# Performance work log

Measured on AMD Instinct MI355X. Metric: run time of the kernel, lower is better.

The kernel has to match this reference:

```python
import jax, jax.numpy as jnp
import numpy as np

B, S, C, D, V = 64, 128, 32, 512, 20000

def setup_inputs() -> dict:
    key = jax.random.key(0)
    ks = jax.random.split(key, 16)
    sc = 1.0 / np.sqrt(D)
    emb = jax.random.normal(ks[0], (V + 1, D), jnp.float32) * 0.02
    emb = emb.at[V].set(0.0)  # padding_idx=-1 -> last row zero
    inp = dict(
        emb=emb,
        W_all_w=jax.random.uniform(ks[1], (4 * D, D), jnp.float32, -sc, sc),
        W_all_b=jnp.zeros((4 * D,), jnp.float32),
        U_all_w=jax.random.uniform(ks[2], (4 * D, D), jnp.float32, -sc, sc),
        U_all_b=jnp.zeros((4 * D,), jnp.float32),
        W_d_w=jax.random.uniform(ks[3], (D, D), jnp.float32, -sc, sc),
        W_d_b=jnp.zeros((D,), jnp.float32),
        sel_w=jax.random.uniform(ks[4], (64, 1), jnp.float32, -1.0, 1.0),
        sel_b=jnp.zeros((64,), jnp.float32),
        time_w=jax.random.uniform(ks[5], (D, 64), jnp.float32, -0.125, 0.125),
        time_b=jnp.zeros((D,), jnp.float32),
        out_w=jax.random.uniform(ks[6], (2, D), jnp.float32, -sc, sc),
        out_b=jnp.zeros((2,), jnp.float32),
        seq_time_step=jax.random.uniform(ks[7], (B, S), jnp.float32, 0.0, 365.0),
        input_seqs=jax.random.randint(ks[8], (B, S, C), 0, V),
        mask=jnp.zeros((B, S), bool),
        lengths=jax.random.randint(ks[9], (B,), 1, S),
        codemask=jnp.zeros((B, S, C), bool),
        label=jax.random.randint(ks[10], (B,), 0, 2),
    )
    return inp


def reference(emb, W_all_w, W_all_b, U_all_w, U_all_b, W_d_w, W_d_b,
              sel_w, sel_b, time_w, time_b, out_w, out_b, seq_time_step,
              input_seqs, mask, lengths, codemask, label):
    # visit embedding: sum code embeddings -> [B,S,D]
    x = emb[input_seqs].sum(axis=2)
    # time feature: 1 - tanh(selection_layer(t/180)^2) -> time_layer -> [B,S,D]
    t = (seq_time_step / 180.0)[..., None]                      # [B,S,1]
    tf = 1.0 - jnp.tanh(jnp.square(t * sel_w[:, 0] + sel_b))    # [B,S,64]
    tf = jnp.einsum('bsk,dk->bsd', tf, time_w) + time_b         # [B,S,D]
    # precompute input projection for all steps: [B,S,4D]
    ux = jnp.einsum('bsd,ed->bse', x, U_all_w) + U_all_b

    def step(carry, inputs):
        h, c = carry
        tf_s, ux_s = inputs                                      # [B,D], [B,4D]
        c_s1 = jnp.tanh(c @ W_d_w.T + W_d_b)
        c_adj = c - c_s1 + c_s1 * tf_s
        outs = h @ W_all_w.T + W_all_b + ux_s
        f, i, o, c_tmp = jnp.split(jax.nn.sigmoid(outs), 4, axis=1)
        c_new = f * c_adj + i * c_tmp
        h_new = o * jnp.tanh(c_new)
        return (h_new, c_new), h_new

    h0 = jnp.zeros((B, D), x.dtype)
    c0 = jnp.zeros((B, D), x.dtype)
    tf_t = jnp.swapaxes(tf, 0, 1)   # [S,B,D]
    ux_t = jnp.swapaxes(ux, 0, 1)   # [S,B,4D]
    _, hs = jax.lax.scan(step, (h0, c0), (tf_t, ux_t))
    outputs = jnp.swapaxes(hs, 0, 1)           # [B,S,D]
    pooled = outputs.max(axis=1)                # MaxPoolLayer without mask
    out = pooled @ out_w.T + out_b              # [B,2]
    return out
```

## Files before the change

kernel.cpp:

```cpp
#include <hip/hip_runtime.h>
#include <hip/hip_bf16.h>

#define B_ 64
#define S_ 128
#define C_ 32
#define D_ 512
#define V_ 20000

typedef float     f32x4  __attribute__((ext_vector_type(4)));
typedef _Float16  f16x8  __attribute__((ext_vector_type(8)));

#define AS1 __attribute__((address_space(1)))
#define AS3 __attribute__((address_space(3)))

#define OFF_XH   0ull
#define OFF_UH   8388608ull
#define OFF_AW   10485760ull
#define OFF_CB   13631488ull
#define OFF_PAD  13639680ull
#define OFF_TWT  13647872ull
#define OFF_EMBH 13778944ull
#define OFF_TF   34259968ull
#define OFF_UX   42648576ull
#define OFF_XB2  76203008ull

#define SENT32 0x7FFF7FFFu

__global__ void k_prep_fused(
    const float* __restrict__ outb, float* __restrict__ outv,
    int4* __restrict__ fillp,
    const float* __restrict__ Wallb, const float* __restrict__ Uallb,
    float* __restrict__ cb,
    const float* __restrict__ tw, float* __restrict__ twt,
    const float* __restrict__ U, _Float16* __restrict__ uh,
    const float* __restrict__ Wall, const float* __restrict__ Wd,
    int4* __restrict__ AW,
    const float* __restrict__ emb, _Float16* __restrict__ eh)
{
    const int blk = blockIdx.x;
    const int t   = threadIdx.x;
    if (blk < 1) {
        if (t < 128) outv[t] = outb[t & 1];
    } else if (blk < 4097) {
        fillp[(blk - 1) * 256 + t] =
            int4{(int)SENT32, (int)SENT32, (int)SENT32, (int)SENT32};
    } else if (blk < 4098) {
        #pragma unroll
        for (int k = 0; k < 8; k++) {
            int i = t * 8 + k;
            cb[i] = Wallb[i] + Uallb[i];
        }
    } else if (blk < 4130) {
        int i2 = (blk - 4098) * 256 + t;
        #pragma unroll
        for (int k = 0; k < 4; k++) {
            int i = i2 * 4 + k;
            twt[(i & 63) * 512 + (i >> 6)] = tw[i];
        }
    } else if (blk < 5154) {
        int i = (blk - 4130) * 256 + t;
        float4 v = ((const float4*)U)[i];
        union { _Float16 h[4]; unsigned long long u; } pk;
        pk.h[0] = (_Float16)v.x; pk.h[1] = (_Float16)v.y;
        pk.h[2] = (_Float16)v.z; pk.h[3] = (_Float16)v.w;
        ((unsigned long long*)uh)[i] = pk.u;
    } else if (blk < 5922) {
        int i = (blk - 5154) * 256 + t;
        int lane = i & 63;  int r = i >> 6;
        int kt = r & 15;    r >>= 4;
        int tile = r % 3;   r /= 3;
        int w = r & 7;      int m = r >> 3;
        int row16 = lane & 15, quad = lane >> 4;
        int q = tile * 2 + (row16 >> 3);
        int d = m * 64 + w * 8 + (row16 & 7);
        int k0 = kt * 32 + quad * 8;
        union { _Float16 h[8]; int4 v; } u;
        const float* src = nullptr;
        if (q < 4)       src = Wall + (size_t)(q * 512 + d) * 512 + k0;
        else if (q == 4) src = Wd   + (size_t)d * 512 + k0;
        #pragma unroll
        for (int j = 0; j < 8; j++) u.h[j] = src ? (_Float16)src[j] : (_Float16)0.f;
        AW[i] = u.v;
    } else {
        int i = (blk - 5922) * 256 + t;
        float2 v = ((const float2*)emb)[i];
        unsigned short hx = __builtin_bit_cast(unsigned short, (_Float16)v.x);
        unsigned short hy = __builtin_bit_cast(unsigned short, (_Float16)v.y);
        ((unsigned*)eh)[i] = (unsigned)hx | ((unsigned)hy << 16);
    }
}

__global__ void k_embed2(const _Float16* __restrict__ embh, const int* __restrict__ seqs,
                         _Float16* __restrict__ xh)
{
    int bs = blockIdx.x;
    int t  = threadIdx.x;
    __shared__ int rows[32];
    if (t < 32) {
        int r = seqs[(size_t)bs * C_ + t];
        rows[t] = (r < 0) ? V_ : r;
    }
    __syncthreads();
    float ax = 0.f, ay = 0.f;
    #pragma unroll 4
    for (int c = 0; c < C_; c++) {
        unsigned v = *(const unsigned*)(embh + (size_t)rows[c] * D_ + 2 * t);
        ax += (float)__builtin_bit_cast(_Float16, (unsigned short)v);
        ay += (float)__builtin_bit_cast(_Float16, (unsigned short)(v >> 16));
    }
    unsigned short hx = __builtin_bit_cast(unsigned short, (_Float16)ax);
    unsigned short hy = __builtin_bit_cast(unsigned short, (_Float16)ay);
    *(unsigned*)(xh + (size_t)bs * D_ + 2 * t) = (unsigned)hx | ((unsigned)hy << 16);
}

__global__ __launch_bounds__(512) void k_tf2(
    const float* __restrict__ stime, const float* __restrict__ selw,
    const float* __restrict__ selb, const float* __restrict__ twT,
    const float* __restrict__ timeb, _Float16* __restrict__ tf)
{
    int bb = blockIdx.x;
    int t  = threadIdx.x;
    __shared__ float s1[16][64];
    for (int idx = t; idx < 1024; idx += 512) {
        int bl = idx >> 6, j = idx & 63;
        float tv = stime[bb * 16 + bl] * (1.0f / 180.0f);
        float u  = tv * selw[j] + selb[j];
        s1[bl][j] = 1.0f - tanhf(u * u);
    }
    __syncthreads();
    int d = t;
    float acc[16];
    float tb = timeb[d];
    #pragma unroll
    for (int l = 0; l < 16; l++) acc[l] = tb;
    for (int j = 0; j < 64; j++) {
        float wj = twT[j * 512 + d];
        #pragma unroll
        for (int l = 0; l < 16; l++) acc[l] = fmaf(s1[l][j], wj, acc[l]);
    }
    #pragma unroll
    for (int l = 0; l < 16; l++)
        tf[(size_t)(bb * 16 + l) * 512 + d] = (_Float16)acc[l];
}

__device__ __forceinline__ void stage16(const _Float16* g, _Float16* l)
{
#if __has_builtin(__builtin_amdgcn_global_load_lds)
    __builtin_amdgcn_global_load_lds((const AS1 void*)g, (AS3 void*)l, 16, 0, 0);
#else
    *(int4*)l = *(const int4*)g;
#endif
}

__global__ __launch_bounds__(256, 4) void k_gemm3(const _Float16* __restrict__ A,
                                                  const _Float16* __restrict__ Bm,
                                                  _Float16* __restrict__ Cg)
{
    __shared__ __align__(16) _Float16 As[128 * 64];
    __shared__ __align__(16) _Float16 Bs[128 * 64];
    const int t = threadIdx.x;
    const int w = t >> 6, lane = t & 63;
    const int wm = w & 1, wn = w >> 1;
    const int m0 = blockIdx.y * 128, n0 = blockIdx.x * 128;
    const int r16 = lane & 15, quad = lane >> 4;

    const int srow = w * 8 + (lane >> 3);
    const int k8g  = (lane & 7) ^ ((lane >> 3) & 7);
    const _Float16* ga = A  + (size_t)(m0 + srow) * 512 + k8g * 8;
    const _Float16* gb = Bm + (size_t)(n0 + srow) * 512 + k8g * 8;
    _Float16* la = As + srow * 64 + (lane & 7) * 8;
    _Float16* lb = Bs + srow * 64 + (lane & 7) * 8;

    f32x4 acc[4][4] = {};
    for (int k0 = 0; k0 < 512; k0 += 64) {
        __syncthreads();
        #pragma unroll
        for (int r = 0; r < 4; r++) {
            stage16(ga + k0 + (size_t)r * 32 * 512, la + r * 32 * 64);
            stage16(gb + k0 + (size_t)r * 32 * 512, lb + r * 32 * 64);
        }
        __syncthreads();
        #pragma unroll
        for (int sub = 0; sub < 2; sub++) {
            f16x8 af[4], bf[4];
            const int ksl = ((sub * 4 + quad) ^ (r16 & 7)) * 8;
            #pragma unroll
            for (int i = 0; i < 4; i++) {
                af[i] = *(const f16x8*)(As + (wm * 64 + i * 16 + r16) * 64 + ksl);
                bf[i] = *(const f16x8*)(Bs + (wn * 64 + i * 16 + r16) * 64 + ksl);
            }
            #pragma unroll
            for (int i = 0; i < 4; i++)
                #pragma unroll
                for (int j = 0; j < 4; j++)
                    acc[i][j] = __builtin_amdgcn_mfma_f32_16x16x32_f16(
                                    af[i], bf[j], acc[i][j], 0, 0, 0);
        }
    }
    #pragma unroll
    for (int i = 0; i < 4; i++)
        #pragma unroll
        for (int j = 0; j < 4; j++) {
            int row = m0 + wm * 64 + i * 16 + quad * 4;
            int col = n0 + wn * 64 + j * 16 + r16;
            _Float16* cp = Cg + (size_t)row * 2048 + col;
            #pragma unroll
            for (int rg = 0; rg < 4; rg++)
                cp[(size_t)rg * 2048] = (_Float16)acc[i][j][rg];
        }
}

__device__ __forceinline__ float fsigm(float x)
{
    return __builtin_amdgcn_rcpf(1.f + __expf(-x));
}
__device__ __forceinline__ float ftanh(float x)
{
    return 1.f - 2.f * __builtin_amdgcn_rcpf(1.f + __expf(2.f * x));
}

__global__ __launch_bounds__(512, 2) void k_rnn7(
    const int4* __restrict__ AW,
    const float* __restrict__ cbv, const float* __restrict__ wdb,
    const _Float16* __restrict__ ux, const _Float16* __restrict__ tf,
    const float* __restrict__ outw,
    float* __restrict__ out,
    unsigned long long* __restrict__ xb64)
{
    const int t    = threadIdx.x;
    const int gid  = blockIdx.x >> 3;
    const int m    = blockIdx.x & 7;
    const int b0   = gid * 2;
    const int w    = t >> 6;
    const int lane = t & 63;
    const int col  = lane & 15;
    const int quad = lane >> 4;

    int4 Af[48];
    {
        const int4* src = AW + (size_t)(m * 8 + w) * 3072;
        #pragma unroll
        for (int i = 0; i < 48; i++) Af[i] = src[i * 64 + lane];
    }

    __shared__ __align__(16) _Float16 xstg[4 * 544];
    __shared__ __align__(16) float cmat[8][4][48];
    __shared__ float pstg[2][64];

    const bool act = (lane < 16);
    const int  pb  = lane >> 3;
    const int  pj  = lane & 7;
    const int  dl  = w * 8 + pj;
    const int  d   = m * 64 + dl;

    float cbf = 0, cbi = 0, cbo = 0, cbc = 0, bdv = 0;
    if (act) {
        cbf = cbv[d]; cbi = cbv[512 + d]; cbo = cbv[1024 + d]; cbc = cbv[1536 + d];
        bdv = wdb[d];
    }
    float c_reg = 0.f, pool = -1e30f;
    const int dw = w * 64 + lane;

    for (int s = 0; s < S_; s++) {
        float uf = 0, ui = 0, uo = 0, uc = 0, tv = 0;
        if (act) {
            size_t bs = (size_t)(b0 + pb) * S_ + s;
            const _Float16* up = ux + bs * 2048 + d;
            uf = (float)up[0];    ui = (float)up[512];
            uo = (float)up[1024]; uc = (float)up[1536];
            tv = (float)tf[bs * 512 + d];
        }

        unsigned long long val = 0ull;
        if (s > 0) {
            const unsigned long long* src =
                xb64 + (((size_t)s * 32 + gid) * 8 + w) * 64 + lane;
            int tries = 0;
            for (;;) {
                val = __hip_atomic_load(src, __ATOMIC_RELAXED,
                                        __HIP_MEMORY_SCOPE_AGENT);
                if ((unsigned)val != SENT32 && (unsigned)(val >> 32) != SENT32)
                    break;
                if (++tries > (1 << 22)) break;
            }
        }
        __syncthreads();
        xstg[0 * 544 + dw] = __builtin_bit_cast(_Float16, (unsigned short)(val));
        xstg[2 * 544 + dw] = __builtin_bit_cast(_Float16, (unsigned short)(val >> 16));
        xstg[1 * 544 + dw] = __builtin_bit_cast(_Float16, (unsigned short)(val >> 32));
        xstg[3 * 544 + dw] = __builtin_bit_cast(_Float16, (unsigned short)(val >> 48));
        __syncthreads();

        f32x4 a0 = {0, 0, 0, 0}, a1 = {0, 0, 0, 0}, a2 = {0, 0, 0, 0};
        #pragma unroll
        for (int kt = 0; kt < 16; kt++) {
            f16x8 b = {};
            if (col < 4)
                b = *(const f16x8*)(xstg + col * 544 + kt * 32 + quad * 8);
            a0 = __builtin_amdgcn_mfma_f32_16x16x32_f16(
                     __builtin_bit_cast(f16x8, Af[kt]),      b, a0, 0, 0, 0);
            a1 = __builtin_amdgcn_mfma_f32_16x16x32_f16(
                     __builtin_bit_cast(f16x8, Af[16 + kt]), b, a1, 0, 0, 0);
            a2 = __builtin_amdgcn_mfma_f32_16x16x32_f16(
                     __builtin_bit_cast(f16x8, Af[32 + kt]), b, a2, 0, 0, 0);
        }

        if (col < 4) {
            *(f32x4*)&cmat[w][col][ 0 + quad * 4] = a0;
            *(f32x4*)&cmat[w][col][16 + quad * 4] = a1;
            *(f32x4*)&cmat[w][col][32 + quad * 4] = a2;
        }

        if (act) {
            float f_  = cmat[w][pb][ 0 + pj];
            float i_  = cmat[w][pb][ 8 + pj];
            float o_  = cmat[w][pb][16 + pj];
            float g_  = cmat[w][pb][24 + pj];
            float wd_ = cmat[w][2 + pb][32 + pj];
            float gf = fsigm(f_ + cbf + uf);
            float gi = fsigm(i_ + cbi + ui);
            float go = fsigm(o_ + cbo + uo);
            float gc = fsigm(g_ + cbc + uc);
            float cs1  = ftanh(wd_ + bdv);
            float cadj = c_reg - cs1 + cs1 * tv;
            float cn   = gf * cadj + gi * gc;
            float hn   = go * ftanh(cn);
            c_reg = cn;
            pool  = fmaxf(pool, hn);
            unsigned hh = __builtin_bit_cast(unsigned short, (_Float16)hn);
            unsigned cc = __builtin_bit_cast(unsigned short, (_Float16)cn);
            unsigned pk = hh | (cc << 16);
            unsigned other = __shfl(pk, lane + 8);
            if (pb == 0 && s != S_ - 1) {
                unsigned long long ov =
                    (unsigned long long)pk | ((unsigned long long)other << 32);
                unsigned long long* dst =
                    xb64 + (((size_t)(s + 1) * 32 + gid) * 8 + m) * 64 + dl;
                __hip_atomic_store(dst, ov, __ATOMIC_RELAXED,
                                   __HIP_MEMORY_SCOPE_AGENT);
            }
        }
    }

    if (act) pstg[pb][dl] = pool;
    __syncthreads();
    if (t < 128) {
        int b = t >> 6, l = t & 63;
        float pv = pstg[b][l];
        int dg = m * 64 + l;
        float p0 = pv * outw[dg], p1 = pv * outw[512 + dg];
        #pragma unroll
        for (int off = 32; off > 0; off >>= 1) {
            p0 += __shfl_down(p0, off);
            p1 += __shfl_down(p1, off);
        }
        if (l == 0) {
            atomicAdd(&out[2 * (b0 + b)],     p0);
            atomicAdd(&out[2 * (b0 + b) + 1], p1);
        }
    }
}

extern "C" void kernel_launch(void* const* d_in, const int* in_sizes, int n_in,
                              void* d_out, int out_size, void* d_ws, size_t ws_size,
                              hipStream_t stream)
{
    const float* emb   = (const float*)d_in[0];
    const float* Wall  = (const float*)d_in[1];
    const float* Wallb = (const float*)d_in[2];
    const float* Uall  = (const float*)d_in[3];
    const float* Uallb = (const float*)d_in[4];
    const float* Wdw   = (const float*)d_in[5];
    const float* Wdb   = (const float*)d_in[6];
    const float* selw  = (const float*)d_in[7];
    const float* selb  = (const float*)d_in[8];
    const float* timew = (const float*)d_in[9];
    const float* timeb = (const float*)d_in[10];
    const float* outw  = (const float*)d_in[11];
    const float* outb  = (const float*)d_in[12];
    const float* stime = (const float*)d_in[13];
    const int*   seqs  = (const int*)d_in[14];
    float* out = (float*)d_out;
    char*  ws  = (char*)d_ws;

    _Float16* xh   = (_Float16*)(ws + OFF_XH);
    _Float16* uh   = (_Float16*)(ws + OFF_UH);
    int4*     aw   = (int4*)(ws + OFF_AW);
    float*    cbp  = (float*)(ws + OFF_CB);
    float*    twt  = (float*)(ws + OFF_TWT);
    _Float16* eh   = (_Float16*)(ws + OFF_EMBH);
    _Float16* tfp  = (_Float16*)(ws + OFF_TF);
    _Float16* uxp  = (_Float16*)(ws + OFF_UX);
    unsigned long long* xb = (unsigned long long*)(ws + OFF_XB2);

    k_prep_fused<<<25923, 256, 0, stream>>>(
        outb, out, (int4*)(ws + OFF_XB2),
        Wallb, Uallb, cbp,
        timew, twt,
        Uall, uh,
        Wall, Wdw, aw,
        emb, eh);
    k_embed2 <<<B_ * S_, 256, 0, stream>>>(eh, seqs, xh);
    k_tf2    <<<512,     512, 0, stream>>>(stime, selw, selb, twt, timeb, tfp);
    k_gemm3  <<<dim3(16, 64), 256, 0, stream>>>(xh, uh, uxp);
    k_rnn7   <<<256,     512, 0, stream>>>(aw, cbp, Wdb, uxp, tfp, outw, out, xb);
}
```

Before: 492.7 us.

## Process eight batch rows per RNN block and prefetch next-step hidden state

The recurrent kernel now handles 8 batch rows per block instead of 2, using all 16 MFMA columns, and launches 64 blocks instead of 256. Each thread issues the next step's cross-block state loads right after publishing its own output, overlapping the spin-wait latency with the tail of the current step. The ux/tf loads move after the barrier. This cuts the number of blocks that must synchronise through global memory and raises MFMA utilisation, at the cost of fewer CUs doing the recurrence and more per-step work per block.

```diff
diff --git a/kernel.cpp b/kernel.cpp
--- a/kernel.cpp
+++ b/kernel.cpp
@@ -219,7 +219,7 @@
     return 1.f - 2.f * __builtin_amdgcn_rcpf(1.f + __expf(2.f * x));
 }
 
-__global__ __launch_bounds__(512, 2) void k_rnn7(
+__global__ __launch_bounds__(512, 2) void k_rnn8(
     const int4* __restrict__ AW,
     const float* __restrict__ cbv, const float* __restrict__ wdb,
     const _Float16* __restrict__ ux, const _Float16* __restrict__ tf,
@@ -228,9 +228,8 @@
     unsigned long long* __restrict__ xb64)
 {
     const int t    = threadIdx.x;
-    const int gid  = blockIdx.x >> 3;
-    const int m    = blockIdx.x & 7;
-    const int b0   = gid * 2;
+    const int gp   = blockIdx.x & 7;
+    const int m    = blockIdx.x >> 3;
     const int w    = t >> 6;
     const int lane = t & 63;
     const int col  = lane & 15;
@@ -238,65 +237,81 @@
 
     int4 Af[48];
     {
-        const int4* src = AW + (size_t)(m * 8 + w) * 3072;
-        #pragma unroll
-        for (int i = 0; i < 48; i++) Af[i] = src[i * 64 + lane];
-    }
-
-    __shared__ __align__(16) _Float16 xstg[4 * 544];
-    __shared__ __align__(16) float cmat[8][4][48];
-    __shared__ float pstg[2][64];
-
-    const bool act = (lane < 16);
-    const int  pb  = lane >> 3;
-    const int  pj  = lane & 7;
-    const int  dl  = w * 8 + pj;
-    const int  d   = m * 64 + dl;
-
-    float cbf = 0, cbi = 0, cbo = 0, cbc = 0, bdv = 0;
-    if (act) {
-        cbf = cbv[d]; cbi = cbv[512 + d]; cbo = cbv[1024 + d]; cbc = cbv[1536 + d];
-        bdv = wdb[d];
-    }
+        const int4* srcA = AW + (size_t)(m * 8 + w) * 3072;
+        #pragma unroll
+        for (int i = 0; i < 48; i++) Af[i] = srcA[i * 64 + lane];
+    }
+
+    __shared__ __align__(16) _Float16 xstg[16 * 552];
+    __shared__ __align__(16) float cmat[8][16][52];
+    __shared__ float pstg[8][64];
+
+    const int pj = lane & 7;
+    const int bl = lane >> 3;
+    const int g  = bl >> 1;
+    const int pb = bl & 1;
+    const int dl = w * 8 + pj;
+    const int d  = m * 64 + dl;
+    const int hc = g * 4 + pb;
+    const int cc = g * 4 + 2 + pb;
+
+    const float cbf = cbv[d],        cbi = cbv[512 + d],
+                cbo = cbv[1024 + d], cbc = cbv[1536 + d];
+    const float bdv = wdb[d];
+
     float c_reg = 0.f, pool = -1e30f;
     const int dw = w * 64 + lane;
 
+    const size_t pbase = (size_t)gp * 2048 + (size_t)w * 64 + lane;
+    const size_t bs_base = (size_t)(gp * 8 + bl) * S_;
+
+    unsigned long long nx0 = 0, nx1 = 0, nx2 = 0, nx3 = 0;
+
     for (int s = 0; s < S_; s++) {
-        float uf = 0, ui = 0, uo = 0, uc = 0, tv = 0;
-        if (act) {
-            size_t bs = (size_t)(b0 + pb) * S_ + s;
-            const _Float16* up = ux + bs * 2048 + d;
-            uf = (float)up[0];    ui = (float)up[512];
-            uo = (float)up[1024]; uc = (float)up[1536];
-            tv = (float)tf[bs * 512 + d];
-        }
-
-        unsigned long long val = 0ull;
+        unsigned long long v0 = 0, v1 = 0, v2 = 0, v3 = 0;
         if (s > 0) {
-            const unsigned long long* src =
-                xb64 + (((size_t)s * 32 + gid) * 8 + w) * 64 + lane;
+            v0 = nx0; v1 = nx1; v2 = nx2; v3 = nx3;
+            const unsigned long long* sp = xb64 + (size_t)s * 16384 + pbase;
             int tries = 0;
-            for (;;) {
-                val = __hip_atomic_load(src, __ATOMIC_RELAXED,
-                                        __HIP_MEMORY_SCOPE_AGENT);
-                if ((unsigned)val != SENT32 && (unsigned)(val >> 32) != SENT32)
-                    break;
+            while (((unsigned)v0 == SENT32 || (unsigned)(v0 >> 32) == SENT32) ||
+                   ((unsigned)v1 == SENT32 || (unsigned)(v1 >> 32) == SENT32) ||
+                   ((unsigned)v2 == SENT32 || (unsigned)(v2 >> 32) == SENT32) ||
+                   ((unsigned)v3 == SENT32 || (unsigned)(v3 >> 32) == SENT32)) {
+                v0 = __hip_atomic_load(sp,        __ATOMIC_RELAXED, __HIP_MEMORY_SCOPE_AGENT);
+                v1 = __hip_atomic_load(sp + 512,  __ATOMIC_RELAXED, __HIP_MEMORY_SCOPE_AGENT);
+                v2 = __hip_atomic_load(sp + 1024, __ATOMIC_RELAXED, __HIP_MEMORY_SCOPE_AGENT);
+                v3 = __hip_atomic_load(sp + 1536, __ATOMIC_RELAXED, __HIP_MEMORY_SCOPE_AGENT);
                 if (++tries > (1 << 22)) break;
             }
         }
         __syncthreads();
-        xstg[0 * 544 + dw] = __builtin_bit_cast(_Float16, (unsigned short)(val));
-        xstg[2 * 544 + dw] = __builtin_bit_cast(_Float16, (unsigned short)(val >> 16));
-        xstg[1 * 544 + dw] = __builtin_bit_cast(_Float16, (unsigned short)(val >> 32));
-        xstg[3 * 544 + dw] = __builtin_bit_cast(_Float16, (unsigned short)(val >> 48));
+        xstg[ 0 * 552 + dw] = __builtin_bit_cast(_Float16, (unsigned short)(v0));
+        xstg[ 2 * 552 + dw] = __builtin_bit_cast(_Float16, (unsigned short)(v0 >> 16));
+        xstg[ 1 * 552 + dw] = __builtin_bit_cast(_Float16, (unsigned short)(v0 >> 32));
+        xstg[ 3 * 552 + dw] = __builtin_bit_cast(_Float16, (unsigned short)(v0 >> 48));
+        xstg[ 4 * 552 + dw] = __builtin_bit_cast(_Float16, (unsigned short)(v1));
+        xstg[ 6 * 552 + dw] = __builtin_bit_cast(_Float16, (unsigned short)(v1 >> 16));
+        xstg[ 5 * 552 + dw] = __builtin_bit_cast(_Float16, (unsigned short)(v1 >> 32));
+        xstg[ 7 * 552 + dw] = __builtin_bit_cast(_Float16, (unsigned short)(v1 >> 48));
+        xstg[ 8 * 552 + dw] = __builtin_bit_cast(_Float16, (unsigned short)(v2));
+        xstg[10 * 552 + dw] = __builtin_bit_cast(_Float16, (unsigned short)(v2 >> 16));
+        xstg[ 9 * 552 + dw] = __builtin_bit_cast(_Float16, (unsigned short)(v2 >> 32));
+        xstg[11 * 552 + dw] = __builtin_bit_cast(_Float16, (unsigned short)(v2 >> 48));
+        xstg[12 * 552 + dw] = __builtin_bit_cast(_Float16, (unsigned short)(v3));
+        xstg[14 * 552 + dw] = __builtin_bit_cast(_Float16, (unsigned short)(v3 >> 16));
+        xstg[13 * 552 + dw] = __builtin_bit_cast(_Float16, (unsigned short)(v3 >> 32));
+        xstg[15 * 552 + dw] = __builtin_bit_cast(_Float16, (unsigned short)(v3 >> 48));
         __syncthreads();
 
+        const _Float16* up = ux + (bs_base + s) * 2048 + d;
+        float uf = (float)up[0],    ui = (float)up[512];
+        float uo = (float)up[1024], uc = (float)up[1536];
+        float tv = (float)tf[(bs_base + s) * 512 + d];
+
         f32x4 a0 = {0, 0, 0, 0}, a1 = {0, 0, 0, 0}, a2 = {0, 0, 0, 0};
         #pragma unroll
         for (int kt = 0; kt < 16; kt++) {
-            f16x8 b = {};
-            if (col < 4)
-                b = *(const f16x8*)(xstg + col * 544 + kt * 32 + quad * 8);
+            f16x8 b = *(const f16x8*)(xstg + col * 552 + kt * 32 + quad * 8);
             a0 = __builtin_amdgcn_mfma_f32_16x16x32_f16(
                      __builtin_bit_cast(f16x8, Af[kt]),      b, a0, 0, 0, 0);
             a1 = __builtin_amdgcn_mfma_f32_16x16x32_f16(
@@ -304,59 +319,60 @@
             a2 = __builtin_amdgcn_mfma_f32_16x16x32_f16(
                      __builtin_bit_cast(f16x8, Af[32 + kt]), b, a2, 0, 0, 0);
         }
-
-        if (col < 4) {
-            *(f32x4*)&cmat[w][col][ 0 + quad * 4] = a0;
-            *(f32x4*)&cmat[w][col][16 + quad * 4] = a1;
-            *(f32x4*)&cmat[w][col][32 + quad * 4] = a2;
-        }
-
-        if (act) {
-            float f_  = cmat[w][pb][ 0 + pj];
-            float i_  = cmat[w][pb][ 8 + pj];
-            float o_  = cmat[w][pb][16 + pj];
-            float g_  = cmat[w][pb][24 + pj];
-            float wd_ = cmat[w][2 + pb][32 + pj];
-            float gf = fsigm(f_ + cbf + uf);
-            float gi = fsigm(i_ + cbi + ui);
-            float go = fsigm(o_ + cbo + uo);
-            float gc = fsigm(g_ + cbc + uc);
-            float cs1  = ftanh(wd_ + bdv);
-            float cadj = c_reg - cs1 + cs1 * tv;
-            float cn   = gf * cadj + gi * gc;
-            float hn   = go * ftanh(cn);
-            c_reg = cn;
-            pool  = fmaxf(pool, hn);
-            unsigned hh = __builtin_bit_cast(unsigned short, (_Float16)hn);
-            unsigned cc = __builtin_bit_cast(unsigned short, (_Float16)cn);
-            unsigned pk = hh | (cc << 16);
-            unsigned other = __shfl(pk, lane + 8);
-            if (pb == 0 && s != S_ - 1) {
-                unsigned long long ov =
-                    (unsigned long long)pk | ((unsigned long long)other << 32);
-                unsigned long long* dst =
-                    xb64 + (((size_t)(s + 1) * 32 + gid) * 8 + m) * 64 + dl;
-                __hip_atomic_store(dst, ov, __ATOMIC_RELAXED,
-                                   __HIP_MEMORY_SCOPE_AGENT);
-            }
-        }
-    }
-
-    if (act) pstg[pb][dl] = pool;
+        *(f32x4*)&cmat[w][col][ 0 + quad * 4] = a0;
+        *(f32x4*)&cmat[w][col][16 + quad * 4] = a1;
+        *(f32x4*)&cmat[w][col][32 + quad * 4] = a2;
+
+        float f_  = cmat[w][hc][ 0 + pj];
+        float i_  = cmat[w][hc][ 8 + pj];
+        float o_  = cmat[w][hc][16 + pj];
+        float g_  = cmat[w][hc][24 + pj];
+        float wd_ = cmat[w][cc][32 + pj];
+        float gf = fsigm(f_ + cbf + uf);
+        float gi = fsigm(i_ + cbi + ui);
+        float go = fsigm(o_ + cbo + uo);
+        float gc = fsigm(g_ + cbc + uc);
+        float cs1  = ftanh(wd_ + bdv);
+        float cadj = c_reg - cs1 + cs1 * tv;
+        float cn   = gf * cadj + gi * gc;
+        float hn   = go * ftanh(cn);
+        c_reg = cn;
+        pool  = fmaxf(pool, hn);
+        unsigned hh  = __builtin_bit_cast(unsigned short, (_Float16)hn);
+        unsigned chn = __builtin_bit_cast(unsigned short, (_Float16)cn);
+        unsigned pk  = hh | (chn << 16);
+        unsigned other = __shfl(pk, lane + 8);
+        if (pb == 0 && s != S_ - 1) {
+            unsigned long long ov =
+                (unsigned long long)pk | ((unsigned long long)other << 32);
+            unsigned long long* dst =
+                xb64 + (((size_t)(s + 1) * 32 + (gp * 4 + g)) * 8 + m) * 64 + dl;
+            __hip_atomic_store(dst, ov, __ATOMIC_RELAXED,
+                               __HIP_MEMORY_SCOPE_AGENT);
+        }
+        if (s + 1 < S_) {
+            const unsigned long long* np = xb64 + (size_t)(s + 1) * 16384 + pbase;
+            nx0 = __hip_atomic_load(np,        __ATOMIC_RELAXED, __HIP_MEMORY_SCOPE_AGENT);
+            nx1 = __hip_atomic_load(np + 512,  __ATOMIC_RELAXED, __HIP_MEMORY_SCOPE_AGENT);
+            nx2 = __hip_atomic_load(np + 1024, __ATOMIC_RELAXED, __HIP_MEMORY_SCOPE_AGENT);
+            nx3 = __hip_atomic_load(np + 1536, __ATOMIC_RELAXED, __HIP_MEMORY_SCOPE_AGENT);
+        }
+    }
+
+    pstg[bl][dl] = pool;
     __syncthreads();
-    if (t < 128) {
-        int b = t >> 6, l = t & 63;
-        float pv = pstg[b][l];
-        int dg = m * 64 + l;
+    {
+        float pv = pstg[w][lane];
+        int dg = m * 64 + lane;
         float p0 = pv * outw[dg], p1 = pv * outw[512 + dg];
         #pragma unroll
         for (int off = 32; off > 0; off >>= 1) {
             p0 += __shfl_down(p0, off);
             p1 += __shfl_down(p1, off);
         }
-        if (l == 0) {
-            atomicAdd(&out[2 * (b0 + b)],     p0);
-            atomicAdd(&out[2 * (b0 + b) + 1], p1);
+        if (lane == 0) {
+            atomicAdd(&out[2 * (gp * 8 + w)],     p0);
+            atomicAdd(&out[2 * (gp * 8 + w) + 1], p1);
         }
     }
 }
@@ -403,5 +419,5 @@
     k_embed2 <<<B_ * S_, 256, 0, stream>>>(eh, seqs, xh);
     k_tf2    <<<512,     512, 0, stream>>>(stime, selw, selb, twt, timeb, tfp);
     k_gemm3  <<<dim3(16, 64), 256, 0, stream>>>(xh, uh, uxp);
-    k_rnn7   <<<256,     512, 0, stream>>>(aw, cbp, Wdb, uxp, tfp, outw, out, xb);
-}
+    k_rnn8   <<<64,      512, 0, stream>>>(aw, cbp, Wdb, uxp, tfp, outw, out, xb);
+}
```

Measured after the change: 623.6 us. 26.6% more time.

## Repartition recurrent kernel: 8 batches per block, 16-row tiles, split-K warps

Applied to the files above, without the earlier changes.

The persistent RNN kernel is repartitioned. Before, each block owned 2 batches and 64 hidden units. Now each block owns 8 batches and 16 hidden units, with 10 warps, each covering one gate tile and one half of K. The MFMA B operand now uses all 16 columns (8 batches × h/c) instead of 4, so fewer wasted MFMA lanes and far fewer weight registers per warp (8 int4 instead of 48). The cost is an extra LDS reduction across the two K halves, wider polling loads of the exchange buffer per step, and one block per CU at 640 threads. The weight prep layout is changed to match, and padding tiles are removed.

```diff
diff --git a/kernel.cpp b/kernel.cpp
--- a/kernel.cpp
+++ b/kernel.cpp
@@ -64,25 +64,23 @@
         pk.h[0] = (_Float16)v.x; pk.h[1] = (_Float16)v.y;
         pk.h[2] = (_Float16)v.z; pk.h[3] = (_Float16)v.w;
         ((unsigned long long*)uh)[i] = pk.u;
-    } else if (blk < 5922) {
+    } else if (blk < 5794) {
         int i = (blk - 5154) * 256 + t;
         int lane = i & 63;  int r = i >> 6;
-        int kt = r & 15;    r >>= 4;
-        int tile = r % 3;   r /= 3;
-        int w = r & 7;      int m = r >> 3;
-        int row16 = lane & 15, quad = lane >> 4;
-        int q = tile * 2 + (row16 >> 3);
-        int d = m * 64 + w * 8 + (row16 & 7);
-        int k0 = kt * 32 + quad * 8;
+        int ktl   = r & 7;  int r2 = r >> 3;
+        int khalf = r2 & 1; int r3 = r2 >> 1;
+        int tile  = r3 % 5; int mm = r3 / 5;
+        int row16 = lane & 15, q4 = lane >> 4;
+        int d  = mm * 16 + row16;
+        int k0 = khalf * 256 + ktl * 32 + q4 * 8;
+        const float* src = (tile < 4) ? (Wall + (size_t)(tile * 512 + d) * 512 + k0)
+                                      : (Wd   + (size_t)d * 512 + k0);
         union { _Float16 h[8]; int4 v; } u;
-        const float* src = nullptr;
-        if (q < 4)       src = Wall + (size_t)(q * 512 + d) * 512 + k0;
-        else if (q == 4) src = Wd   + (size_t)d * 512 + k0;
-        #pragma unroll
-        for (int j = 0; j < 8; j++) u.h[j] = src ? (_Float16)src[j] : (_Float16)0.f;
+        #pragma unroll
+        for (int j = 0; j < 8; j++) u.h[j] = (_Float16)src[j];
         AW[i] = u.v;
     } else {
-        int i = (blk - 5922) * 256 + t;
+        int i = (blk - 5794) * 256 + t;
         float2 v = ((const float2*)emb)[i];
         unsigned short hx = __builtin_bit_cast(unsigned short, (_Float16)v.x);
         unsigned short hy = __builtin_bit_cast(unsigned short, (_Float16)v.y);
@@ -219,7 +217,7 @@
     return 1.f - 2.f * __builtin_amdgcn_rcpf(1.f + __expf(2.f * x));
 }
 
-__global__ __launch_bounds__(512, 2) void k_rnn7(
+__global__ __launch_bounds__(640, 1) void k_rnn9(
     const int4* __restrict__ AW,
     const float* __restrict__ cbv, const float* __restrict__ wdb,
     const _Float16* __restrict__ ux, const _Float16* __restrict__ tf,
@@ -228,95 +226,101 @@
     unsigned long long* __restrict__ xb64)
 {
     const int t    = threadIdx.x;
-    const int gid  = blockIdx.x >> 3;
-    const int m    = blockIdx.x & 7;
-    const int b0   = gid * 2;
+    const int g    = blockIdx.x >> 5;
+    const int mm   = blockIdx.x & 31;
     const int w    = t >> 6;
     const int lane = t & 63;
     const int col  = lane & 15;
     const int quad = lane >> 4;
-
-    int4 Af[48];
+    const int tile = w >> 1, khalf = w & 1;
+
+    int4 Af[8];
     {
-        const int4* src = AW + (size_t)(m * 8 + w) * 3072;
-        #pragma unroll
-        for (int i = 0; i < 48; i++) Af[i] = src[i * 64 + lane];
-    }
-
-    __shared__ __align__(16) _Float16 xstg[4 * 544];
-    __shared__ __align__(16) float cmat[8][4][48];
-    __shared__ float pstg[2][64];
-
-    const bool act = (lane < 16);
-    const int  pb  = lane >> 3;
-    const int  pj  = lane & 7;
-    const int  dl  = w * 8 + pj;
-    const int  d   = m * 64 + dl;
+        const int4* src = AW + (size_t)(((mm * 5 + tile) * 2 + khalf) * 8) * 64;
+        #pragma unroll
+        for (int i = 0; i < 8; i++) Af[i] = src[i * 64 + lane];
+    }
+
+    __shared__ __align__(16) _Float16 xstg[16 * 520];
+    __shared__ __align__(16) float cmat[5][2][16][20];
+
+    const bool act = (t < 128);
+    const int bl   = t >> 4;
+    const int d16  = t & 15;
+    const int gg   = bl >> 1, pb = bl & 1;
+    const int dg   = mm * 16 + d16;
+    const int batch = g * 8 + bl;
+    const int hcol = gg * 4 + pb;
+    const int ccol = gg * 4 + 2 + pb;
 
     float cbf = 0, cbi = 0, cbo = 0, cbc = 0, bdv = 0;
     if (act) {
-        cbf = cbv[d]; cbi = cbv[512 + d]; cbo = cbv[1024 + d]; cbc = cbv[1536 + d];
-        bdv = wdb[d];
+        cbf = cbv[dg]; cbi = cbv[512 + dg]; cbo = cbv[1024 + dg]; cbc = cbv[1536 + dg];
+        bdv = wdb[dg];
     }
     float c_reg = 0.f, pool = -1e30f;
-    const int dw = w * 64 + lane;
+
+    const bool stg = (t < 512);
+    const int  k0  = (t * 4) & 511;
+    const int  sgg = t >> 7;
+    const size_t pboff = (size_t)g * 2048 + (size_t)t * 4;
 
     for (int s = 0; s < S_; s++) {
-        float uf = 0, ui = 0, uo = 0, uc = 0, tv = 0;
-        if (act) {
-            size_t bs = (size_t)(b0 + pb) * S_ + s;
-            const _Float16* up = ux + bs * 2048 + d;
-            uf = (float)up[0];    ui = (float)up[512];
-            uo = (float)up[1024]; uc = (float)up[1536];
-            tv = (float)tf[bs * 512 + d];
-        }
-
-        unsigned long long val = 0ull;
-        if (s > 0) {
-            const unsigned long long* src =
-                xb64 + (((size_t)s * 32 + gid) * 8 + w) * 64 + lane;
+        unsigned long long v0 = 0, v1 = 0, v2 = 0, v3 = 0;
+        if (stg && s > 0) {
+            const unsigned long long* sp = xb64 + (size_t)s * 16384 + pboff;
             int tries = 0;
             for (;;) {
-                val = __hip_atomic_load(src, __ATOMIC_RELAXED,
-                                        __HIP_MEMORY_SCOPE_AGENT);
-                if ((unsigned)val != SENT32 && (unsigned)(val >> 32) != SENT32)
+                v0 = __hip_atomic_load(sp + 0, __ATOMIC_RELAXED, __HIP_MEMORY_SCOPE_AGENT);
+                v1 = __hip_atomic_load(sp + 1, __ATOMIC_RELAXED, __HIP_MEMORY_SCOPE_AGENT);
+                v2 = __hip_atomic_load(sp + 2, __ATOMIC_RELAXED, __HIP_MEMORY_SCOPE_AGENT);
+                v3 = __hip_atomic_load(sp + 3, __ATOMIC_RELAXED, __HIP_MEMORY_SCOPE_AGENT);
+                if ((unsigned)v0 != SENT32 && (unsigned)v1 != SENT32 &&
+                    (unsigned)v2 != SENT32 && (unsigned)v3 != SENT32)
                     break;
                 if (++tries > (1 << 22)) break;
             }
         }
+        if (stg) {
+            unsigned long long h0 = (v0 & 0xFFFFull)         | ((v1 & 0xFFFFull) << 16)
+                                  | ((v2 & 0xFFFFull) << 32) | ((v3 & 0xFFFFull) << 48);
+            unsigned long long c0 = ((v0 >> 16) & 0xFFFFull)         | (((v1 >> 16) & 0xFFFFull) << 16)
+                                  | (((v2 >> 16) & 0xFFFFull) << 32) | (((v3 >> 16) & 0xFFFFull) << 48);
+            unsigned long long h1 = ((v0 >> 32) & 0xFFFFull)         | (((v1 >> 32) & 0xFFFFull) << 16)
+                                  | (((v2 >> 32) & 0xFFFFull) << 32) | (((v3 >> 32) & 0xFFFFull) << 48);
+            unsigned long long c1 = (v0 >> 48)          | ((v1 >> 48) << 16)
+                                  | ((v2 >> 48) << 32)  | ((v3 >> 48) << 48);
+            *(unsigned long long*)(xstg + (sgg * 4 + 0) * 520 + k0) = h0;
+            *(unsigned long long*)(xstg + (sgg * 4 + 1) * 520 + k0) = h1;
+            *(unsigned long long*)(xstg + (sgg * 4 + 2) * 520 + k0) = c0;
+            *(unsigned long long*)(xstg + (sgg * 4 + 3) * 520 + k0) = c1;
+        }
         __syncthreads();
-        xstg[0 * 544 + dw] = __builtin_bit_cast(_Float16, (unsigned short)(val));
-        xstg[2 * 544 + dw] = __builtin_bit_cast(_Float16, (unsigned short)(val >> 16));
-        xstg[1 * 544 + dw] = __builtin_bit_cast(_Float16, (unsigned short)(val >> 32));
-        xstg[3 * 544 + dw] = __builtin_bit_cast(_Float16, (unsigned short)(val >> 48));
+
+        float uf = 0, ui = 0, uo = 0, uc = 0, tv = 0;
+        if (act) {
+            const _Float16* up = ux + ((size_t)batch * S_ + s) * 2048 + dg;
+            uf = (float)up[0];    ui = (float)up[512];
+            uo = (float)up[1024]; uc = (float)up[1536];
+            tv = (float)tf[((size_t)batch * S_ + s) * 512 + dg];
+        }
+
+        f32x4 a = {0, 0, 0, 0};
+        #pragma unroll
+        for (int kt = 0; kt < 8; kt++) {
+            f16x8 b = *(const f16x8*)(xstg + col * 520 + (khalf * 8 + kt) * 32 + quad * 8);
+            a = __builtin_amdgcn_mfma_f32_16x16x32_f16(
+                    __builtin_bit_cast(f16x8, Af[kt]), b, a, 0, 0, 0);
+        }
+        *(f32x4*)&cmat[tile][khalf][col][quad * 4] = a;
         __syncthreads();
 
-        f32x4 a0 = {0, 0, 0, 0}, a1 = {0, 0, 0, 0}, a2 = {0, 0, 0, 0};
-        #pragma unroll
-        for (int kt = 0; kt < 16; kt++) {
-            f16x8 b = {};
-            if (col < 4)
-                b = *(const f16x8*)(xstg + col * 544 + kt * 32 + quad * 8);
-            a0 = __builtin_amdgcn_mfma_f32_16x16x32_f16(
-                     __builtin_bit_cast(f16x8, Af[kt]),      b, a0, 0, 0, 0);
-            a1 = __builtin_amdgcn_mfma_f32_16x16x32_f16(
-                     __builtin_bit_cast(f16x8, Af[16 + kt]), b, a1, 0, 0, 0);
-            a2 = __builtin_amdgcn_mfma_f32_16x16x32_f16(
-                     __builtin_bit_cast(f16x8, Af[32 + kt]), b, a2, 0, 0, 0);
-        }
-
-        if (col < 4) {
-            *(f32x4*)&cmat[w][col][ 0 + quad * 4] = a0;
-            *(f32x4*)&cmat[w][col][16 + quad * 4] = a1;
-            *(f32x4*)&cmat[w][col][32 + quad * 4] = a2;
-        }
-
         if (act) {
-            float f_  = cmat[w][pb][ 0 + pj];
-            float i_  = cmat[w][pb][ 8 + pj];
-            float o_  = cmat[w][pb][16 + pj];
-            float g_  = cmat[w][pb][24 + pj];
-            float wd_ = cmat[w][2 + pb][32 + pj];
+            float f_  = cmat[0][0][hcol][d16] + cmat[0][1][hcol][d16];
+            float i_  = cmat[1][0][hcol][d16] + cmat[1][1][hcol][d16];
+            float o_  = cmat[2][0][hcol][d16] + cmat[2][1][hcol][d16];
+            float g_  = cmat[3][0][hcol][d16] + cmat[3][1][hcol][d16];
+            float wd_ = cmat[4][0][ccol][d16] + cmat[4][1][ccol][d16];
             float gf = fsigm(f_ + cbf + uf);
             float gi = fsigm(i_ + cbi + ui);
             float go = fsigm(o_ + cbo + uo);
@@ -327,36 +331,31 @@
             float hn   = go * ftanh(cn);
             c_reg = cn;
             pool  = fmaxf(pool, hn);
-            unsigned hh = __builtin_bit_cast(unsigned short, (_Float16)hn);
-            unsigned cc = __builtin_bit_cast(unsigned short, (_Float16)cn);
-            unsigned pk = hh | (cc << 16);
-            unsigned other = __shfl(pk, lane + 8);
+            unsigned hh  = __builtin_bit_cast(unsigned short, (_Float16)hn);
+            unsigned chn = __builtin_bit_cast(unsigned short, (_Float16)cn);
+            unsigned pk  = hh | (chn << 16);
+            unsigned other = __shfl(pk, lane + 16);
             if (pb == 0 && s != S_ - 1) {
                 unsigned long long ov =
                     (unsigned long long)pk | ((unsigned long long)other << 32);
                 unsigned long long* dst =
-                    xb64 + (((size_t)(s + 1) * 32 + gid) * 8 + m) * 64 + dl;
+                    xb64 + (size_t)(s + 1) * 16384 + (size_t)(g * 4 + gg) * 512 + dg;
                 __hip_atomic_store(dst, ov, __ATOMIC_RELAXED,
                                    __HIP_MEMORY_SCOPE_AGENT);
             }
         }
     }
 
-    if (act) pstg[pb][dl] = pool;
-    __syncthreads();
-    if (t < 128) {
-        int b = t >> 6, l = t & 63;
-        float pv = pstg[b][l];
-        int dg = m * 64 + l;
-        float p0 = pv * outw[dg], p1 = pv * outw[512 + dg];
-        #pragma unroll
-        for (int off = 32; off > 0; off >>= 1) {
-            p0 += __shfl_down(p0, off);
-            p1 += __shfl_down(p1, off);
-        }
-        if (l == 0) {
-            atomicAdd(&out[2 * (b0 + b)],     p0);
-            atomicAdd(&out[2 * (b0 + b) + 1], p1);
+    if (act) {
+        float p0 = pool * outw[dg], p1 = pool * outw[512 + dg];
+        #pragma unroll
+        for (int off = 8; off > 0; off >>= 1) {
+            p0 += __shfl_down(p0, off, 16);
+            p1 += __shfl_down(p1, off, 16);
+        }
+        if (d16 == 0) {
+            atomicAdd(&out[2 * batch],     p0);
+            atomicAdd(&out[2 * batch + 1], p1);
         }
     }
 }
@@ -393,7 +392,7 @@
     _Float16* uxp  = (_Float16*)(ws + OFF_UX);
     unsigned long long* xb = (unsigned long long*)(ws + OFF_XB2);
 
-    k_prep_fused<<<25923, 256, 0, stream>>>(
+    k_prep_fused<<<25795, 256, 0, stream>>>(
         outb, out, (int4*)(ws + OFF_XB2),
         Wallb, Uallb, cbp,
         timew, twt,
@@ -403,5 +402,5 @@
     k_embed2 <<<B_ * S_, 256, 0, stream>>>(eh, seqs, xh);
     k_tf2    <<<512,     512, 0, stream>>>(stime, selw, selb, twt, timeb, tfp);
     k_gemm3  <<<dim3(16, 64), 256, 0, stream>>>(xh, uh, uxp);
-    k_rnn7   <<<256,     512, 0, stream>>>(aw, cbp, Wdb, uxp, tfp, outw, out, xb);
-}
+    k_rnn9   <<<256,     640, 0, stream>>>(aw, cbp, Wdb, uxp, tfp, outw, out, xb);
+}
```

New measurement: 648.4 us. 1.32x slower.

## Give each wave a private staging buffer and drop per-step block barriers

Applied to the files above, without the earlier changes.

Each wave now polls and loads the full hidden/cell state vector for its batch pair on its own (8 atomic 64-bit loads per lane) into a per-wave LDS buffer. This removes both __syncthreads per timestep in the recurrent loop. The exchange layout is changed so producers pack four consecutive h values and four c values into two 64-bit stores, and the cmat row indexing is updated to match. The cost is eight times more global polling traffic per block, plus extra shuffles to pack the values.

```diff
diff --git a/kernel.cpp b/kernel.cpp
--- a/kernel.cpp
+++ b/kernel.cpp
@@ -219,7 +219,7 @@
     return 1.f - 2.f * __builtin_amdgcn_rcpf(1.f + __expf(2.f * x));
 }
 
-__global__ __launch_bounds__(512, 2) void k_rnn7(
+__global__ __launch_bounds__(512, 2) void k_rnn10(
     const int4* __restrict__ AW,
     const float* __restrict__ cbv, const float* __restrict__ wdb,
     const _Float16* __restrict__ ux, const _Float16* __restrict__ tf,
@@ -243,8 +243,8 @@
         for (int i = 0; i < 48; i++) Af[i] = src[i * 64 + lane];
     }
 
-    __shared__ __align__(16) _Float16 xstg[4 * 544];
-    __shared__ __align__(16) float cmat[8][4][48];
+    __shared__ __align__(16) _Float16 xstg[8][4 * 528];
+    __shared__ float cmat[8][4][48];
     __shared__ float pstg[2][64];
 
     const bool act = (lane < 16);
@@ -259,9 +259,38 @@
         bdv = wdb[d];
     }
     float c_reg = 0.f, pool = -1e30f;
-    const int dw = w * 64 + lane;
+
+    const int sl = lane >> 4;
+    const int ql = lane & 15;
+    _Float16* xw = xstg[w];
+
+    const int qi = m * 16 + w * 2 + (pj >> 2);
 
     for (int s = 0; s < S_; s++) {
+        unsigned long long v0 = 0, v1 = 0, v2 = 0, v3 = 0,
+                           v4 = 0, v5 = 0, v6 = 0, v7 = 0;
+        if (s > 0) {
+            const unsigned long long* sp =
+                xb64 + ((size_t)s * 32 + gid) * 512 + ql * 4 + sl;
+            int tries = 0;
+            for (;;) {
+                v0 = __hip_atomic_load(sp + 0 * 64, __ATOMIC_RELAXED, __HIP_MEMORY_SCOPE_AGENT);
+                v1 = __hip_atomic_load(sp + 1 * 64, __ATOMIC_RELAXED, __HIP_MEMORY_SCOPE_AGENT);
+                v2 = __hip_atomic_load(sp + 2 * 64, __ATOMIC_RELAXED, __HIP_MEMORY_SCOPE_AGENT);
+                v3 = __hip_atomic_load(sp + 3 * 64, __ATOMIC_RELAXED, __HIP_MEMORY_SCOPE_AGENT);
+                v4 = __hip_atomic_load(sp + 4 * 64, __ATOMIC_RELAXED, __HIP_MEMORY_SCOPE_AGENT);
+                v5 = __hip_atomic_load(sp + 5 * 64, __ATOMIC_RELAXED, __HIP_MEMORY_SCOPE_AGENT);
+                v6 = __hip_atomic_load(sp + 6 * 64, __ATOMIC_RELAXED, __HIP_MEMORY_SCOPE_AGENT);
+                v7 = __hip_atomic_load(sp + 7 * 64, __ATOMIC_RELAXED, __HIP_MEMORY_SCOPE_AGENT);
+                if ((unsigned)v0 != SENT32 && (unsigned)v1 != SENT32 &&
+                    (unsigned)v2 != SENT32 && (unsigned)v3 != SENT32 &&
+                    (unsigned)v4 != SENT32 && (unsigned)v5 != SENT32 &&
+                    (unsigned)v6 != SENT32 && (unsigned)v7 != SENT32)
+                    break;
+                if (++tries > (1 << 22)) break;
+            }
+        }
+
         float uf = 0, ui = 0, uo = 0, uc = 0, tv = 0;
         if (act) {
             size_t bs = (size_t)(b0 + pb) * S_ + s;
@@ -271,32 +300,24 @@
             tv = (float)tf[bs * 512 + d];
         }
 
-        unsigned long long val = 0ull;
-        if (s > 0) {
-            const unsigned long long* src =
-                xb64 + (((size_t)s * 32 + gid) * 8 + w) * 64 + lane;
-            int tries = 0;
-            for (;;) {
-                val = __hip_atomic_load(src, __ATOMIC_RELAXED,
-                                        __HIP_MEMORY_SCOPE_AGENT);
-                if ((unsigned)val != SENT32 && (unsigned)(val >> 32) != SENT32)
-                    break;
-                if (++tries > (1 << 22)) break;
-            }
-        }
-        __syncthreads();
-        xstg[0 * 544 + dw] = __builtin_bit_cast(_Float16, (unsigned short)(val));
-        xstg[2 * 544 + dw] = __builtin_bit_cast(_Float16, (unsigned short)(val >> 16));
-        xstg[1 * 544 + dw] = __builtin_bit_cast(_Float16, (unsigned short)(val >> 32));
-        xstg[3 * 544 + dw] = __builtin_bit_cast(_Float16, (unsigned short)(val >> 48));
-        __syncthreads();
+        {
+            _Float16* xwb = xw + sl * 528 + ql * 4;
+            *(unsigned long long*)(xwb + 0 * 64) = v0;
+            *(unsigned long long*)(xwb + 1 * 64) = v1;
+            *(unsigned long long*)(xwb + 2 * 64) = v2;
+            *(unsigned long long*)(xwb + 3 * 64) = v3;
+            *(unsigned long long*)(xwb + 4 * 64) = v4;
+            *(unsigned long long*)(xwb + 5 * 64) = v5;
+            *(unsigned long long*)(xwb + 6 * 64) = v6;
+            *(unsigned long long*)(xwb + 7 * 64) = v7;
+        }
 
         f32x4 a0 = {0, 0, 0, 0}, a1 = {0, 0, 0, 0}, a2 = {0, 0, 0, 0};
         #pragma unroll
         for (int kt = 0; kt < 16; kt++) {
             f16x8 b = {};
             if (col < 4)
-                b = *(const f16x8*)(xstg + col * 544 + kt * 32 + quad * 8);
+                b = *(const f16x8*)(xw + col * 528 + kt * 32 + quad * 8);
             a0 = __builtin_amdgcn_mfma_f32_16x16x32_f16(
                      __builtin_bit_cast(f16x8, Af[kt]),      b, a0, 0, 0, 0);
             a1 = __builtin_amdgcn_mfma_f32_16x16x32_f16(
@@ -312,11 +333,11 @@
         }
 
         if (act) {
-            float f_  = cmat[w][pb][ 0 + pj];
-            float i_  = cmat[w][pb][ 8 + pj];
-            float o_  = cmat[w][pb][16 + pj];
-            float g_  = cmat[w][pb][24 + pj];
-            float wd_ = cmat[w][2 + pb][32 + pj];
+            float f_  = cmat[w][2 * pb][ 0 + pj];
+            float i_  = cmat[w][2 * pb][ 8 + pj];
+            float o_  = cmat[w][2 * pb][16 + pj];
+            float g_  = cmat[w][2 * pb][24 + pj];
+            float wd_ = cmat[w][2 * pb + 1][32 + pj];
             float gf = fsigm(f_ + cbf + uf);
             float gi = fsigm(i_ + cbi + ui);
             float go = fsigm(o_ + cbo + uo);
@@ -329,14 +350,24 @@
             pool  = fmaxf(pool, hn);
             unsigned hh = __builtin_bit_cast(unsigned short, (_Float16)hn);
             unsigned cc = __builtin_bit_cast(unsigned short, (_Float16)cn);
-            unsigned pk = hh | (cc << 16);
-            unsigned other = __shfl(pk, lane + 8);
-            if (pb == 0 && s != S_ - 1) {
-                unsigned long long ov =
-                    (unsigned long long)pk | ((unsigned long long)other << 32);
+            unsigned h1 = __shfl(hh, lane + 1), h2 = __shfl(hh, lane + 2),
+                     h3 = __shfl(hh, lane + 3);
+            unsigned c1 = __shfl(cc, lane + 1), c2 = __shfl(cc, lane + 2),
+                     c3 = __shfl(cc, lane + 3);
+            if ((pj & 3) == 0 && s != S_ - 1) {
+                unsigned long long hq = (unsigned long long)hh
+                    | ((unsigned long long)h1 << 16)
+                    | ((unsigned long long)h2 << 32)
+                    | ((unsigned long long)h3 << 48);
+                unsigned long long cq = (unsigned long long)cc
+                    | ((unsigned long long)c1 << 16)
+                    | ((unsigned long long)c2 << 32)
+                    | ((unsigned long long)c3 << 48);
                 unsigned long long* dst =
-                    xb64 + (((size_t)(s + 1) * 32 + gid) * 8 + m) * 64 + dl;
-                __hip_atomic_store(dst, ov, __ATOMIC_RELAXED,
+                    xb64 + ((size_t)(s + 1) * 32 + gid) * 512 + qi * 4 + 2 * pb;
+                __hip_atomic_store(dst,     hq, __ATOMIC_RELAXED,
+                                   __HIP_MEMORY_SCOPE_AGENT);
+                __hip_atomic_store(dst + 1, cq, __ATOMIC_RELAXED,
                                    __HIP_MEMORY_SCOPE_AGENT);
             }
         }
@@ -403,5 +434,5 @@
     k_embed2 <<<B_ * S_, 256, 0, stream>>>(eh, seqs, xh);
     k_tf2    <<<512,     512, 0, stream>>>(stime, selw, selb, twt, timeb, tfp);
     k_gemm3  <<<dim3(16, 64), 256, 0, stream>>>(xh, uh, uxp);
-    k_rnn7   <<<256,     512, 0, stream>>>(aw, cbp, Wdb, uxp, tfp, outw, out, xb);
-}
+    k_rnn10  <<<256,     512, 0, stream>>>(aw, cbp, Wdb, uxp, tfp, outw, out, xb);
+}
```

Result: slower. 775.6 us (+57.4%).
